# Optimization experiments

Measured on AMD Instinct MI355X. Metric: run time of the kernel, lower is better.

The kernel has to match this reference:

```python
import jax, jax.numpy as jnp
import numpy as np

B, T, C, H = 8, 1024, 1024, 16
HD = C // H  # head dim = 64
NEG = -1e9


def setup_inputs() -> dict:
    key = jax.random.key(0)
    ks = jax.random.split(key, 10)
    total = B * T
    x = jax.random.normal(ks[0], (total, C), dtype=jnp.float32)
    # identity pack: each padded row is a contiguous chunk of tokens
    padpack_index = jnp.arange(total, dtype=jnp.int64).reshape(B, T)
    # sorted per-row sequence ids -> block-diagonal attention within each packed row
    padpack_batch = jnp.sort(jax.random.randint(ks[1], (B, T), 0, 4, dtype=jnp.int32), axis=-1)
    padpack_inverse_index = jnp.arange(total, dtype=jnp.int64)
    s = 1.0 / np.sqrt(C)
    Wq = jax.random.uniform(ks[2], (C, C), jnp.float32, -s, s)
    bq = jax.random.uniform(ks[3], (C,), jnp.float32, -s, s)
    Wk = jax.random.uniform(ks[4], (C, C), jnp.float32, -s, s)
    bk = jax.random.uniform(ks[5], (C,), jnp.float32, -s, s)
    Wv = jax.random.uniform(ks[6], (C, C), jnp.float32, -s, s)
    bv = jax.random.uniform(ks[7], (C,), jnp.float32, -s, s)
    Wp = jax.random.uniform(ks[8], (C, C), jnp.float32, -s, s)
    bp = jax.random.uniform(ks[9], (C,), jnp.float32, -s, s)
    return {"x": x, "padpack_index": padpack_index, "padpack_batch": padpack_batch,
            "padpack_inverse_index": padpack_inverse_index,
            "Wq": Wq, "bq": bq, "Wk": Wk, "bk": bk, "Wv": Wv, "bv": bv, "Wp": Wp, "bp": bp}


def reference(x, padpack_index, padpack_batch, padpack_inverse_index,
              Wq, bq, Wk, bk, Wv, bv, Wp, bp):
    # gather ragged tokens into padded [B, T, C]
    xp = x[padpack_index]
    # torch Linear: y = x @ W.T + b
    q = (xp @ Wq.T + bq).reshape(B, T, H, HD)
    k = (xp @ Wk.T + bk).reshape(B, T, H, HD)
    v = (xp @ Wv.T + bv).reshape(B, T, H, HD)
    scale = 1.0 / np.sqrt(HD).astype(np.float32)
    att = jnp.einsum('bihd,bjhd->bhij', q, k) * scale  # [B,H,T,T]
    # mask: token pairs from different packed sequences cannot attend
    mask = (padpack_batch[:, :, None] != padpack_batch[:, None, :])[:, None]  # [B,1,T,T]
    att = jnp.where(mask, NEG, att)
    att = jax.nn.softmax(att, axis=-1)
    y = jnp.einsum('bhij,bjhd->bihd', att, v).reshape(B, T, C)
    y = y @ Wp.T + bp
    # scatter back to ragged layout [total_tokens, C]
    return y.reshape(B * T, C)[padpack_inverse_index]
```

## Files before the change

### kernel.cpp

```cpp
#include <hip/hip_runtime.h>


typedef __attribute__((ext_vector_type(8))) short short8;
typedef __attribute__((ext_vector_type(4))) float f32x4;

#define MFMA16(a, b, c) __builtin_amdgcn_mfma_f32_16x16x32_bf16((a), (b), (c), 0, 0, 0)

__device__ __forceinline__ ushort f2b(float f) {
  union { float f; unsigned u; } v; v.f = f;
  unsigned u = v.u;
  return (ushort)((u + 0x7fffu + ((u >> 16) & 1u)) >> 16);
}

__device__ __forceinline__ void gload16(const void* g, void* l) {
  __builtin_amdgcn_global_load_lds((const __attribute__((address_space(1))) unsigned int*)g,
                                   (__attribute__((address_space(3))) unsigned int*)l,
                                   16, 0, 0);
}

__device__ __forceinline__ void cvt4(const float* __restrict__ s, ushort* __restrict__ d) {
  const float4 v = *(const float4*)s;
  ushort4 r; r.x = f2b(v.x); r.y = f2b(v.y); r.z = f2b(v.z); r.w = f2b(v.w);
  *(ushort4*)d = r;
}

__global__ __launch_bounds__(256) void prep(const float* __restrict__ x,
    const float* __restrict__ wq, const float* __restrict__ wk,
    const float* __restrict__ wv, const float* __restrict__ wp,
    ushort* __restrict__ xb, ushort* __restrict__ wb,
    const int* __restrict__ pb, int* __restrict__ bnd) {
  const int bid = blockIdx.x;
  if (bid >= 2048) {
    const int b = bid - 2048;
    const int* p = pb + b * 1024;
    const int i = threadIdx.x;
#pragma unroll
    for (int e = 0; e < 4; ++e) {
      const int idx = i * 4 + e;
      const int cur = p[idx];
      const int prev = (idx == 0) ? -1 : p[idx - 1];
      for (int v = prev + 1; v <= cur; ++v) bnd[b * 8 + v] = idx;
    }
    if (i == 255) {
      const int cur = p[1023];
      for (int v = cur + 1; v <= 4; ++v) bnd[b * 8 + v] = 1024;
    }
    return;
  }
  const long long NX = 8388608ll;
#pragma unroll
  for (int it = 0; it < 6; ++it) {
    const long long e0 = (((long long)(it * 2048 + bid)) * 256 + threadIdx.x) * 4;
    if (e0 < NX) {
      cvt4(x + e0, xb + e0);
    } else {
      const long long t = e0 - NX;
      const int sel = (int)(t >> 20);
      const float* w = sel == 0 ? wq : sel == 1 ? wk : sel == 2 ? wv : wp;
      cvt4(w + (t & 1048575), wb + t);
    }
  }
}

template <int MODE>
__global__ __launch_bounds__(512, 2) void gemm8(
    const ushort* __restrict__ A, const ushort* __restrict__ Bw,
    const float* __restrict__ bias0, const float* __restrict__ bias1,
    const float* __restrict__ bias2,
    ushort* __restrict__ O0, ushort* __restrict__ O1, ushort* __restrict__ O2,
    float* __restrict__ Of) {
  constexpr int ACH = 256 * 64;
  constexpr int BCH = 128 * 64;
  constexpr int BUFB = 2 * (ACH + BCH);
  __shared__ __align__(16) char smem[3 * BUFB];

  const int tid = threadIdx.x, lane = tid & 63, wid = tid >> 6;
  const int wr = wid >> 1, wc = wid & 1;
  const int lg = lane >> 4, lc = lane & 15;

  const int id = blockIdx.x;
  const int s = id >> 3;
  const int m0 = ((id & 7) * 4 + (s & 3)) << 8;
  const int n0 = (s >> 2) << 7;

  f32x4 acc[4][4] = {};

  const int sr0 = tid >> 2;
  const int sc0 = (tid & 3) ^ ((sr0 >> 1) & 3);

#define STAGE(dst_, kh, kt) { \
    char* ad = (dst_) + (kh) * ACH; \
    char* bd = (dst_) + 2 * ACH + (kh) * BCH; \
    const int kcol = (kt) * 64 + (kh) * 32; \
    gload16(A + (size_t)(m0 + sr0) * 1024 + kcol + sc0 * 8, ad + tid * 16); \
    gload16(A + (size_t)(m0 + 128 + sr0) * 1024 + kcol + sc0 * 8, ad + (tid + 512) * 16); \
    gload16(Bw + (size_t)(n0 + sr0) * 1024 + kcol + sc0 * 8, bd + tid * 16); \
  }

#define PHASE_COMPUTE(src_, kh) { \
    const char* ab = (src_) + (kh) * ACH; \
    const char* bb = (src_) + 2 * ACH + (kh) * BCH; \
    short8 af[4]; short8 bf[4]; \
    _Pragma("unroll") \
    for (int f = 0; f < 4; ++f) { \
      const int row = wr * 64 + f * 16 + lc; \
      af[f] = *(const short8*)(ab + row * 64 + ((lg ^ ((row >> 1) & 3)) << 4)); \
    } \
    _Pragma("unroll") \
    for (int g = 0; g < 4; ++g) { \
      const int row = wc * 64 + g * 16 + lc; \
      bf[g] = *(const short8*)(bb + row * 64 + ((lg ^ ((row >> 1) & 3)) << 4)); \
    } \
    __builtin_amdgcn_s_setprio(1); \
    _Pragma("unroll") \
    for (int f = 0; f < 4; ++f) \
      _Pragma("unroll") \
      for (int g = 0; g < 4; ++g) \
        acc[f][g] = MFMA16(af[f], bf[g], acc[f][g]); \
    __builtin_amdgcn_s_setprio(0); \
  }

#define WAITVM(n) { asm volatile("s_waitcnt vmcnt(" #n ")" ::: "memory"); }
#define BARF() { __builtin_amdgcn_s_barrier(); asm volatile("" ::: "memory"); }

  char* b0 = smem;
  char* b1 = smem + BUFB;
  char* b2 = smem + 2 * BUFB;

  STAGE(b0, 0, 0)
  STAGE(b0, 1, 0)
  STAGE(b1, 0, 1)
  STAGE(b1, 1, 1)

  for (int t = 0; t < 14; ++t) {
    WAITVM(9)
    BARF()
    STAGE(b2, 0, t + 2)
    PHASE_COMPUTE(b0, 0)
    WAITVM(9)
    BARF()
    STAGE(b2, 1, t + 2)
    PHASE_COMPUTE(b0, 1)
    char* tmp = b0; b0 = b1; b1 = b2; b2 = tmp;
  }
  WAITVM(9)
  BARF()
  PHASE_COMPUTE(b0, 0)
  WAITVM(6)
  BARF()
  PHASE_COMPUTE(b0, 1)
  WAITVM(3)
  BARF()
  PHASE_COMPUTE(b1, 0)
  WAITVM(0)
  BARF()
  PHASE_COMPUTE(b1, 1)

  if constexpr (MODE == 0) {
    const int sel = n0 >> 10, nloc = n0 & 1023;
    const float* bias = sel == 0 ? bias0 : sel == 1 ? bias1 : bias2;
    float bval[4];
#pragma unroll
    for (int g = 0; g < 4; ++g) bval[g] = bias[nloc + wc * 64 + g * 16 + lc];
    if (sel < 2) {
      ushort* dst = sel ? O1 : O0;
#pragma unroll
      for (int f = 0; f < 4; ++f)
#pragma unroll
        for (int j = 0; j < 4; ++j) {
          const size_t row = m0 + wr * 64 + f * 16 + lg * 4 + j;
#pragma unroll
          for (int g = 0; g < 4; ++g)
            dst[row * 1024 + nloc + wc * 64 + g * 16 + lc] = f2b(acc[f][g][j] + bval[g]);
        }
    } else {
      ushort (*Ts)[136] = (ushort(*)[136])smem;
#pragma unroll
      for (int mh = 0; mh < 2; ++mh) {
        __syncthreads();
        if ((wr >> 1) == mh) {
#pragma unroll
          for (int f = 0; f < 4; ++f)
#pragma unroll
            for (int g = 0; g < 4; ++g)
#pragma unroll
              for (int j = 0; j < 4; ++j)
                Ts[(wr & 1) * 64 + f * 16 + lg * 4 + j][wc * 64 + g * 16 + lc] =
                    f2b(acc[f][g][j] + bval[g]);
        }
        __syncthreads();
        const int c = tid >> 2;
        const int th = (tid & 3) * 32;
        const int gt = m0 + mh * 128;
        const int b = gt >> 10;
        const int t0 = (gt & 1023) + th;
        const int gc = nloc + c;
        ushort* dp = O2 + ((size_t)((b * 16 + (gc >> 6)) * 64 + (gc & 63))) * 1024 + t0;
#pragma unroll
        for (int gb = 0; gb < 4; ++gb) {
          short8 pk;
#pragma unroll
          for (int u = 0; u < 8; ++u) pk[u] = (short)Ts[th + gb * 8 + u][c];
          *(short8*)(dp + gb * 8) = pk;
        }
      }
    }
  } else {
    float bval[4];
#pragma unroll
    for (int g = 0; g < 4; ++g) bval[g] = bias0[n0 + wc * 64 + g * 16 + lc];
#pragma unroll
    for (int f = 0; f < 4; ++f)
#pragma unroll
      for (int j = 0; j < 4; ++j) {
        const size_t row = m0 + wr * 64 + f * 16 + lg * 4 + j;
#pragma unroll
        for (int g = 0; g < 4; ++g)
          Of[row * 1024 + n0 + wc * 64 + g * 16 + lc] = acc[f][g][j] + bval[g];
      }
  }
#undef STAGE
#undef PHASE_COMPUTE
#undef WAITVM
#undef BARF
}

__global__ __launch_bounds__(512) void attn(const ushort* __restrict__ Q,
    const ushort* __restrict__ K, const ushort* __restrict__ Vt,
    const int* __restrict__ bnd, ushort* __restrict__ O) {
  __shared__ __align__(16) char kvbuf[2][16384];
  __shared__ __align__(16) ushort Plds[8][16][68];

  const int tid = threadIdx.x, lane = tid & 63, w = tid >> 6;
  const int lg = lane >> 4, lc = lane & 15;

  const int id = blockIdx.x;
  const int xcd = id & 7, slot = id >> 3;
  const int bh = xcd + 8 * (slot >> 3);
  const int qt = slot & 7;
  const int b = bh >> 4, h = bh & 15;
  const int q0 = qt * 128 + w * 16;

  const int* bd = bnd + b * 8;
  const int b1 = bd[1], b2 = bd[2], b3 = bd[3], b4 = bd[4];
#define SEGID(k) (((k) >= b1) + ((k) >= b2) + ((k) >= b3) + ((k) >= b4))

  const int qid = SEGID(q0 + lc);
  int klo_l = (qid > 0) ? b1 : 0;
  klo_l = (qid > 1) ? b2 : klo_l;
  klo_l = (qid > 2) ? b3 : klo_l;
  int khi_l = (qid > 0) ? b2 : b1;
  khi_l = (qid > 1) ? b3 : khi_l;
  khi_l = (qid > 2) ? b4 : khi_l;

  const int bq_lo = SEGID(qt * 128), bq_hi = SEGID(qt * 128 + 127);
  unsigned am = 0;
#pragma unroll
  for (int jt = 0; jt < 16; ++jt) {
    const int tlo = SEGID(jt * 64), thi = SEGID(jt * 64 + 63);
    if (thi >= bq_lo && tlo <= bq_hi) am |= (1u << jt);
  }

  const ushort* qp = Q + (size_t)(b * 1024 + q0 + lc) * 1024 + h * 64 + lg * 8;
  const short8 qf0 = *(const short8*)qp;
  const short8 qf1 = *(const short8*)(qp + 32);

  const int r0 = tid >> 3;
  const int c16 = (tid & 7) ^ (r0 & 7);
  const ushort* Kg = K + (size_t)(b * 1024 + r0) * 1024 + h * 64 + c16 * 8;
  const ushort* Vg = Vt + (size_t)(bh * 64 + r0) * 1024 + c16 * 8;

#define STAGE(bufp, j) { \
    gload16(Kg + (size_t)(j) * 1024, (bufp) + tid * 16); \
    gload16(Vg + (j), (bufp) + 8192 + tid * 16); }

#define SOFF(r, ch) ((r) * 128 + ((((ch) ^ ((r) & 7))) << 4))

  float mr = -1e30f, lr = 0.f;
  f32x4 o[4] = {};

  unsigned rem = am;
  int jc = __builtin_ctz(rem) * 64;
  rem &= rem - 1;
  STAGE(kvbuf[0], jc)
  __syncthreads();
  int cur = 0;

  for (;;) {
    int jn = -1;
    if (rem) {
      jn = __builtin_ctz(rem) * 64;
      rem &= rem - 1;
      STAGE(kvbuf[cur ^ 1], jn)
    }
    const char* bufK = kvbuf[cur];
    const char* bufV = kvbuf[cur] + 8192;

    short8 kf[8];
#pragma unroll
    for (int n = 0; n < 4; ++n) {
      const int rr = n * 16 + lc;
      kf[2 * n] = *(const short8*)(bufK + SOFF(rr, lg));
      kf[2 * n + 1] = *(const short8*)(bufK + SOFF(rr, lg + 4));
    }
    f32x4 s[4];
    __builtin_amdgcn_s_setprio(1);
#pragma unroll
    for (int n = 0; n < 4; ++n) {
      f32x4 z = {};
      z = MFMA16(kf[2 * n], qf0, z);
      s[n] = MFMA16(kf[2 * n + 1], qf1, z);
    }
    __builtin_amdgcn_s_setprio(0);

#pragma unroll
    for (int n = 0; n < 4; ++n) {
      const int kk = jc + n * 16 + lg * 4;
#pragma unroll
      for (int r = 0; r < 4; ++r) {
        const bool ok = (kk + r >= klo_l) && (kk + r < khi_l);
        s[n][r] = ok ? s[n][r] * 0.125f : -1e9f;
      }
    }

    float rm = fmaxf(fmaxf(fmaxf(s[0][0], s[0][1]), fmaxf(s[0][2], s[0][3])),
                     fmaxf(fmaxf(fmaxf(s[1][0], s[1][1]), fmaxf(s[1][2], s[1][3])),
                           fmaxf(fmaxf(fmaxf(s[2][0], s[2][1]), fmaxf(s[2][2], s[2][3])),
                                 fmaxf(fmaxf(s[3][0], s[3][1]), fmaxf(s[3][2], s[3][3])))));
    rm = fmaxf(rm, __shfl_xor(rm, 16));
    rm = fmaxf(rm, __shfl_xor(rm, 32));
    float mn = mr;
    if (!__all(rm <= mr + 8.f)) {
      mn = fmaxf(mr, rm);
      const float sf = __expf(mr - mn);
      mr = mn;
      lr *= sf;
      const float s0 = __shfl(sf, lg * 4 + 0);
      const float s1 = __shfl(sf, lg * 4 + 1);
      const float s2 = __shfl(sf, lg * 4 + 2);
      const float s3 = __shfl(sf, lg * 4 + 3);
#pragma unroll
      for (int n = 0; n < 4; ++n) {
        o[n][0] *= s0; o[n][1] *= s1; o[n][2] *= s2; o[n][3] *= s3;
      }
    }
    float rs = 0.f;
#pragma unroll
    for (int n = 0; n < 4; ++n)
#pragma unroll
      for (int r = 0; r < 4; ++r) {
        const float p = __expf(s[n][r] - mn);
        s[n][r] = p; rs += p;
      }
    rs += __shfl_xor(rs, 16);
    rs += __shfl_xor(rs, 32);
    lr += rs;

#pragma unroll
    for (int n = 0; n < 4; ++n) {
      ushort4 pk;
      pk.x = f2b(s[n][0]); pk.y = f2b(s[n][1]); pk.z = f2b(s[n][2]); pk.w = f2b(s[n][3]);
      *(ushort4*)&Plds[w][lc][n * 16 + lg * 4] = pk;
    }
    asm volatile("s_waitcnt lgkmcnt(0)" ::: "memory");
    __builtin_amdgcn_sched_barrier(0);
    const short8 p0 = *(const short8*)&Plds[w][lc][lg * 8];
    const short8 p1 = *(const short8*)&Plds[w][lc][32 + lg * 8];
    __builtin_amdgcn_sched_barrier(0);

    short8 vv[8];
#pragma unroll
    for (int n = 0; n < 4; ++n) {
      const int rr = n * 16 + lc;
      vv[2 * n] = *(const short8*)(bufV + SOFF(rr, lg));
      vv[2 * n + 1] = *(const short8*)(bufV + SOFF(rr, lg + 4));
    }
    __builtin_amdgcn_s_setprio(1);
#pragma unroll
    for (int n = 0; n < 4; ++n) {
      o[n] = MFMA16(p0, vv[2 * n], o[n]);
      o[n] = MFMA16(p1, vv[2 * n + 1], o[n]);
    }
    __builtin_amdgcn_s_setprio(0);

    if (jn < 0) break;
    __syncthreads();
    cur ^= 1;
    jc = jn;
  }

  const float linv = 1.f / lr;
  const float i0 = __shfl(linv, lg * 4 + 0);
  const float i1 = __shfl(linv, lg * 4 + 1);
  const float i2 = __shfl(linv, lg * 4 + 2);
  const float i3 = __shfl(linv, lg * 4 + 3);
#pragma unroll
  for (int n = 0; n < 4; ++n) {
    const size_t base = (size_t)(b * 1024 + q0) * 1024 + h * 64 + n * 16 + lc;
    O[base + 0 * 1024 + (size_t)lg * 4096] = f2b(o[n][0] * i0);
    O[base + 1 * 1024 + (size_t)lg * 4096] = f2b(o[n][1] * i1);
    O[base + 2 * 1024 + (size_t)lg * 4096] = f2b(o[n][2] * i2);
    O[base + 3 * 1024 + (size_t)lg * 4096] = f2b(o[n][3] * i3);
  }
#undef STAGE
#undef SOFF
#undef SEGID
}

extern "C" void kernel_launch(void* const* d_in, const int* in_sizes, int n_in,
                              void* d_out, int out_size, void* d_ws, size_t ws_size,
                              hipStream_t stream) {
  const float* x  = (const float*)d_in[0];
  const int*  pb  = (const int*)d_in[2];
  const float* Wq = (const float*)d_in[4]; const float* bq = (const float*)d_in[5];
  const float* Wk = (const float*)d_in[6]; const float* bk = (const float*)d_in[7];
  const float* Wv = (const float*)d_in[8]; const float* bv = (const float*)d_in[9];
  const float* Wp = (const float*)d_in[10]; const float* bp = (const float*)d_in[11];
  float* out = (float*)d_out;
  char* ws = (char*)d_ws;

  ushort* xb = (ushort*)ws;
  ushort* wb = (ushort*)(ws + (16u << 20));
  ushort* Qb = (ushort*)(ws + (24u << 20));
  ushort* Kb = (ushort*)(ws + (40u << 20));
  ushort* Vt = (ushort*)(ws + (56u << 20));
  int*    bnd = (int*)(ws + (72u << 20));
  ushort* Ob = xb;

  prep<<<2056, 256, 0, stream>>>(x, Wq, Wk, Wv, Wp, xb, wb, pb, bnd);
  gemm8<0><<<768, 512, 0, stream>>>(xb, wb, bq, bk, bv, Qb, Kb, Vt, nullptr);
  attn<<<1024, 512, 0, stream>>>(Qb, Kb, Vt, bnd, Ob);
  gemm8<1><<<256, 512, 0, stream>>>(Ob, wb + (3 << 20), bp,
                                    nullptr, nullptr, nullptr, nullptr, nullptr, out);
}
```

Measured before the change: 148.3 us.

## Fuse x fp32-to-bf16 conversion into QKV GEMM A-tile loading

The prep kernel no longer converts x to bf16. Instead a new QKV GEMM reads fp32 x directly into registers, converts it with packed bf16 conversion instructions, and stores it into a swizzled LDS slot. It uses a three-slot rotating buffer with direct-to-LDS loads for the weights. This removes a full write and re-read of the 16 MB bf16 x copy, at the cost of twice the global A traffic per tile and extra VALU and register work inside the GEMM main loop. The GEMM is re-specialized into separate QKV and projection kernels.

Result: slower. 161.8 us (+9.1%).

```diff
diff --git a/kernel.cpp b/kernel.cpp
--- a/kernel.cpp
+++ b/kernel.cpp
@@ -24,14 +24,23 @@
   *(ushort4*)d = r;
 }
 
-__global__ __launch_bounds__(256) void prep(const float* __restrict__ x,
+__device__ __forceinline__ void cvt_store16(float4 a, float4 b, void* dst) {
+  unsigned r0, r1, r2, r3;
+  asm("v_cvt_pk_bf16_f32 %0, %1, %2" : "=v"(r0) : "v"(a.x), "v"(a.y));
+  asm("v_cvt_pk_bf16_f32 %0, %1, %2" : "=v"(r1) : "v"(a.z), "v"(a.w));
+  asm("v_cvt_pk_bf16_f32 %0, %1, %2" : "=v"(r2) : "v"(b.x), "v"(b.y));
+  asm("v_cvt_pk_bf16_f32 %0, %1, %2" : "=v"(r3) : "v"(b.z), "v"(b.w));
+  uint4 w; w.x = r0; w.y = r1; w.z = r2; w.w = r3;
+  *(uint4*)dst = w;
+}
+
+__global__ __launch_bounds__(256) void prep_w(
     const float* __restrict__ wq, const float* __restrict__ wk,
     const float* __restrict__ wv, const float* __restrict__ wp,
-    ushort* __restrict__ xb, ushort* __restrict__ wb,
-    const int* __restrict__ pb, int* __restrict__ bnd) {
+    ushort* __restrict__ wb, const int* __restrict__ pb, int* __restrict__ bnd) {
   const int bid = blockIdx.x;
-  if (bid >= 2048) {
-    const int b = bid - 2048;
+  if (bid >= 1024) {
+    const int b = bid - 1024;
     const int* p = pb + b * 1024;
     const int i = threadIdx.x;
 #pragma unroll
@@ -47,28 +56,169 @@
     }
     return;
   }
-  const long long NX = 8388608ll;
-#pragma unroll
-  for (int it = 0; it < 6; ++it) {
-    const long long e0 = (((long long)(it * 2048 + bid)) * 256 + threadIdx.x) * 4;
-    if (e0 < NX) {
-      cvt4(x + e0, xb + e0);
-    } else {
-      const long long t = e0 - NX;
-      const int sel = (int)(t >> 20);
-      const float* w = sel == 0 ? wq : sel == 1 ? wk : sel == 2 ? wv : wp;
-      cvt4(w + (t & 1048575), wb + t);
-    }
-  }
-}
-
-template <int MODE>
-__global__ __launch_bounds__(512, 2) void gemm8(
+#pragma unroll
+  for (int it = 0; it < 4; ++it) {
+    const long long t = (((long long)(it * 1024 + bid)) * 256 + threadIdx.x) * 4;
+    const int sel = (int)(t >> 20);
+    const float* w = sel == 0 ? wq : sel == 1 ? wk : sel == 2 ? wv : wp;
+    cvt4(w + (t & 1048575), wb + t);
+  }
+}
+
+__global__ __launch_bounds__(512, 2) void gemm_qkvF(
+    const float* __restrict__ X, const ushort* __restrict__ Bw,
+    const float* __restrict__ bq, const float* __restrict__ bk, const float* __restrict__ bv,
+    ushort* __restrict__ Qb, ushort* __restrict__ Kb, ushort* __restrict__ Vt) {
+  constexpr int ASL = 16384;
+  constexpr int SLOT = ASL + 8192;
+  __shared__ __align__(16) char smem[3 * SLOT];
+
+  const int tid = threadIdx.x, lane = tid & 63, wid = tid >> 6;
+  const int wr = wid >> 1, wc = wid & 1;
+  const int lg = lane >> 4, lc = lane & 15;
+
+  const int id = blockIdx.x;
+  const int s = id >> 3;
+  const int m0 = ((id & 7) * 4 + (s & 3)) << 8;
+  const int n0 = (s >> 2) << 7;
+
+  f32x4 acc[4][4] = {};
+
+  const int sr0 = tid >> 2;
+  const int sc0 = (tid & 3) ^ ((sr0 >> 1) & 3);
+  const float*  ax0 = X + (size_t)(m0 + sr0) * 1024 + sc0 * 8;
+  const float*  ax1 = ax0 + (size_t)128 * 1024;
+  const ushort* bx  = Bw + (size_t)(n0 + sr0) * 1024 + sc0 * 8;
+
+  float4 ar0, ar1, ar2, ar3;
+
+#define AISSUE(c) { \
+    const float* s0_ = ax0 + (c) * 32; \
+    const float* s1_ = ax1 + (c) * 32; \
+    ar0 = *(const float4*)s0_; ar1 = *(const float4*)(s0_ + 4); \
+    ar2 = *(const float4*)s1_; ar3 = *(const float4*)(s1_ + 4); }
+
+#define ACVT(slot_) { \
+    cvt_store16(ar0, ar1, (slot_) + tid * 16); \
+    cvt_store16(ar2, ar3, (slot_) + (tid + 512) * 16); }
+
+#define BISSUE(c, slot_) { gload16(bx + (size_t)(c) * 32, (slot_) + ASL + tid * 16); }
+
+#define COMPUTE(slot_) { \
+    const char* ab = (slot_); \
+    const char* bb = (slot_) + ASL; \
+    short8 af[4]; short8 bf[4]; \
+    _Pragma("unroll") \
+    for (int f = 0; f < 4; ++f) { \
+      const int row = wr * 64 + f * 16 + lc; \
+      af[f] = *(const short8*)(ab + row * 64 + ((lg ^ ((row >> 1) & 3)) << 4)); \
+    } \
+    _Pragma("unroll") \
+    for (int g = 0; g < 4; ++g) { \
+      const int row = wc * 64 + g * 16 + lc; \
+      bf[g] = *(const short8*)(bb + row * 64 + ((lg ^ ((row >> 1) & 3)) << 4)); \
+    } \
+    __builtin_amdgcn_s_setprio(1); \
+    _Pragma("unroll") \
+    for (int f = 0; f < 4; ++f) \
+      _Pragma("unroll") \
+      for (int g = 0; g < 4; ++g) \
+        acc[f][g] = MFMA16(af[f], bf[g], acc[f][g]); \
+    __builtin_amdgcn_s_setprio(0); \
+  }
+
+#define WAITVM(n) { asm volatile("s_waitcnt vmcnt(" #n ")" ::: "memory"); }
+#define LGKMBAR() { asm volatile("s_waitcnt lgkmcnt(0)" ::: "memory"); \
+                    __builtin_amdgcn_s_barrier(); \
+                    asm volatile("" ::: "memory"); }
+
+  char* pc = smem;
+  char* pw = smem + SLOT;
+  char* pi = smem + 2 * SLOT;
+
+  AISSUE(0)
+  BISSUE(0, pc)
+  LGKMBAR()
+  ACVT(pc)
+  AISSUE(1)
+  BISSUE(1, pw)
+
+  for (int c = 2; c < 32; ++c) {
+    WAITVM(5)
+    LGKMBAR()
+    ACVT(pw)
+    AISSUE(c)
+    BISSUE(c, pi)
+    COMPUTE(pc)
+    char* t_ = pc; pc = pw; pw = pi; pi = t_;
+  }
+  WAITVM(5)
+  LGKMBAR()
+  ACVT(pw)
+  COMPUTE(pc)
+  WAITVM(0)
+  LGKMBAR()
+  COMPUTE(pw)
+
+  const int sel = n0 >> 10, nloc = n0 & 1023;
+  const float* bias = sel == 0 ? bq : sel == 1 ? bk : bv;
+  float bval[4];
+#pragma unroll
+  for (int g = 0; g < 4; ++g) bval[g] = bias[nloc + wc * 64 + g * 16 + lc];
+  if (sel < 2) {
+    ushort* dst = sel ? Kb : Qb;
+#pragma unroll
+    for (int f = 0; f < 4; ++f)
+#pragma unroll
+      for (int j = 0; j < 4; ++j) {
+        const size_t row = m0 + wr * 64 + f * 16 + lg * 4 + j;
+#pragma unroll
+        for (int g = 0; g < 4; ++g)
+          dst[row * 1024 + nloc + wc * 64 + g * 16 + lc] = f2b(acc[f][g][j] + bval[g]);
+      }
+  } else {
+    ushort (*Ts)[136] = (ushort(*)[136])smem;
+#pragma unroll
+    for (int mh = 0; mh < 2; ++mh) {
+      __syncthreads();
+      if ((wr >> 1) == mh) {
+#pragma unroll
+        for (int f = 0; f < 4; ++f)
+#pragma unroll
+          for (int g = 0; g < 4; ++g)
+#pragma unroll
+            for (int j = 0; j < 4; ++j)
+              Ts[(wr & 1) * 64 + f * 16 + lg * 4 + j][wc * 64 + g * 16 + lc] =
+                  f2b(acc[f][g][j] + bval[g]);
+      }
+      __syncthreads();
+      const int c = tid >> 2;
+      const int th = (tid & 3) * 32;
+      const int gt = m0 + mh * 128;
+      const int b = gt >> 10;
+      const int t0 = (gt & 1023) + th;
+      const int gc = nloc + c;
+      ushort* dp = Vt + ((size_t)((b * 16 + (gc >> 6)) * 64 + (gc & 63))) * 1024 + t0;
+#pragma unroll
+      for (int gb = 0; gb < 4; ++gb) {
+        short8 pk;
+#pragma unroll
+        for (int u = 0; u < 8; ++u) pk[u] = (short)Ts[th + gb * 8 + u][c];
+        *(short8*)(dp + gb * 8) = pk;
+      }
+    }
+  }
+#undef AISSUE
+#undef ACVT
+#undef BISSUE
+#undef COMPUTE
+#undef WAITVM
+#undef LGKMBAR
+}
+
+__global__ __launch_bounds__(512, 2) void gemm_proj(
     const ushort* __restrict__ A, const ushort* __restrict__ Bw,
-    const float* __restrict__ bias0, const float* __restrict__ bias1,
-    const float* __restrict__ bias2,
-    ushort* __restrict__ O0, ushort* __restrict__ O1, ushort* __restrict__ O2,
-    float* __restrict__ Of) {
+    const float* __restrict__ bias0, float* __restrict__ Of) {
   constexpr int ACH = 256 * 64;
   constexpr int BCH = 128 * 64;
   constexpr int BUFB = 2 * (ACH + BCH);
@@ -156,69 +306,18 @@
   BARF()
   PHASE_COMPUTE(b1, 1)
 
-  if constexpr (MODE == 0) {
-    const int sel = n0 >> 10, nloc = n0 & 1023;
-    const float* bias = sel == 0 ? bias0 : sel == 1 ? bias1 : bias2;
-    float bval[4];
-#pragma unroll
-    for (int g = 0; g < 4; ++g) bval[g] = bias[nloc + wc * 64 + g * 16 + lc];
-    if (sel < 2) {
-      ushort* dst = sel ? O1 : O0;
-#pragma unroll
-      for (int f = 0; f < 4; ++f)
-#pragma unroll
-        for (int j = 0; j < 4; ++j) {
-          const size_t row = m0 + wr * 64 + f * 16 + lg * 4 + j;
-#pragma unroll
-          for (int g = 0; g < 4; ++g)
-            dst[row * 1024 + nloc + wc * 64 + g * 16 + lc] = f2b(acc[f][g][j] + bval[g]);
-        }
-    } else {
-      ushort (*Ts)[136] = (ushort(*)[136])smem;
-#pragma unroll
-      for (int mh = 0; mh < 2; ++mh) {
-        __syncthreads();
-        if ((wr >> 1) == mh) {
-#pragma unroll
-          for (int f = 0; f < 4; ++f)
-#pragma unroll
-            for (int g = 0; g < 4; ++g)
-#pragma unroll
-              for (int j = 0; j < 4; ++j)
-                Ts[(wr & 1) * 64 + f * 16 + lg * 4 + j][wc * 64 + g * 16 + lc] =
-                    f2b(acc[f][g][j] + bval[g]);
-        }
-        __syncthreads();
-        const int c = tid >> 2;
-        const int th = (tid & 3) * 32;
-        const int gt = m0 + mh * 128;
-        const int b = gt >> 10;
-        const int t0 = (gt & 1023) + th;
-        const int gc = nloc + c;
-        ushort* dp = O2 + ((size_t)((b * 16 + (gc >> 6)) * 64 + (gc & 63))) * 1024 + t0;
-#pragma unroll
-        for (int gb = 0; gb < 4; ++gb) {
-          short8 pk;
-#pragma unroll
-          for (int u = 0; u < 8; ++u) pk[u] = (short)Ts[th + gb * 8 + u][c];
-          *(short8*)(dp + gb * 8) = pk;
-        }
-      }
-    }
-  } else {
-    float bval[4];
-#pragma unroll
-    for (int g = 0; g < 4; ++g) bval[g] = bias0[n0 + wc * 64 + g * 16 + lc];
-#pragma unroll
-    for (int f = 0; f < 4; ++f)
-#pragma unroll
-      for (int j = 0; j < 4; ++j) {
-        const size_t row = m0 + wr * 64 + f * 16 + lg * 4 + j;
-#pragma unroll
-        for (int g = 0; g < 4; ++g)
-          Of[row * 1024 + n0 + wc * 64 + g * 16 + lc] = acc[f][g][j] + bval[g];
-      }
-  }
+  float bval[4];
+#pragma unroll
+  for (int g = 0; g < 4; ++g) bval[g] = bias0[n0 + wc * 64 + g * 16 + lc];
+#pragma unroll
+  for (int f = 0; f < 4; ++f)
+#pragma unroll
+    for (int j = 0; j < 4; ++j) {
+      const size_t row = m0 + wr * 64 + f * 16 + lg * 4 + j;
+#pragma unroll
+      for (int g = 0; g < 4; ++g)
+        Of[row * 1024 + n0 + wc * 64 + g * 16 + lc] = acc[f][g][j] + bval[g];
+    }
 #undef STAGE
 #undef PHASE_COMPUTE
 #undef WAITVM
@@ -419,17 +518,15 @@
   float* out = (float*)d_out;
   char* ws = (char*)d_ws;
 
-  ushort* xb = (ushort*)ws;
+  ushort* Ob = (ushort*)ws;
   ushort* wb = (ushort*)(ws + (16u << 20));
   ushort* Qb = (ushort*)(ws + (24u << 20));
   ushort* Kb = (ushort*)(ws + (40u << 20));
   ushort* Vt = (ushort*)(ws + (56u << 20));
   int*    bnd = (int*)(ws + (72u << 20));
-  ushort* Ob = xb;
-
-  prep<<<2056, 256, 0, stream>>>(x, Wq, Wk, Wv, Wp, xb, wb, pb, bnd);
-  gemm8<0><<<768, 512, 0, stream>>>(xb, wb, bq, bk, bv, Qb, Kb, Vt, nullptr);
+
+  prep_w<<<1032, 256, 0, stream>>>(Wq, Wk, Wv, Wp, wb, pb, bnd);
+  gemm_qkvF<<<768, 512, 0, stream>>>(x, wb, bq, bk, bv, Qb, Kb, Vt);
   attn<<<1024, 512, 0, stream>>>(Qb, Kb, Vt, bnd, Ob);
-  gemm8<1><<<256, 512, 0, stream>>>(Ob, wb + (3 << 20), bp,
-                                    nullptr, nullptr, nullptr, nullptr, nullptr, out);
-}
+  gemm_proj<<<256, 512, 0, stream>>>(Ob, wb + (3 << 20), bp, out);
+}
```
